# Kernel optimization log

Hardware: AMD Instinct MI355X
Metric: run time of the kernel (lower is better)

Reference implementation:

```python
import jax, jax.numpy as jnp
import numpy as np

B, M, N = 1, 8192, 131072      # batch, bones, window points
C_BOT, C = 16, 128             # bottleneck_channel, channel
K_MAX, FOLD, R_UP = 8, 8, 4    # max neighbors, fold_channel, upsample rate r
EPS = 1e-8


def _lin_init(key, fan_in, fan_out):
    return jax.random.normal(key, (fan_in, fan_out), jnp.float32) / np.sqrt(fan_in)


def setup_inputs() -> dict:
    key = jax.random.key(0)
    ks = jax.random.split(key, 10)
    return {
        "quantized_cf": jax.random.normal(ks[0], (B, M, C_BOT), jnp.float32),
        "d_idx": jax.random.randint(ks[1], (B, N, K_MAX), 0, M),
        "d_windows": jax.random.normal(ks[2], (B, N, 3), jnp.float32),
        "bones": jax.random.normal(ks[3], (B, M, 3), jnp.float32),
        "K": 8,
        # fea_stretch Linear(bottleneck -> channel)
        "W_stretch": _lin_init(ks[4], C_BOT, C),
        "b_stretch": jnp.zeros((C,), jnp.float32),
        # DWUS folding MLP: (C+3) -> C -> FOLD*R_UP -> 3 (per fold point)
        "W1": _lin_init(ks[5], C + 3, C),
        "b1": jnp.zeros((C,), jnp.float32),
        "W2": _lin_init(ks[6], C, FOLD * R_UP),
        "b2": jnp.zeros((FOLD * R_UP,), jnp.float32),
        "W3": _lin_init(ks[7], FOLD, 3),
        "b3": jnp.zeros((3,), jnp.float32),
    }


def reference(quantized_cf, d_idx, d_windows, bones, K,
              W_stretch, b_stretch, W1, b1, W2, b2, W3, b3):
    # fea_stretch: per-bone feature expansion  [B, M, C]
    skin_fea = jnp.einsum("bmc,cd->bmd", quantized_cf, W_stretch) + b_stretch

    idx = d_idx[..., :K]                                   # [B, N, K]
    batch = jnp.arange(B)[:, None, None]
    g_fea = skin_fea[batch, idx]                           # [B, N, K, C] gather
    g_bones = bones[batch, idx]                            # [B, N, K, 3]

    # inverse-distance interpolation of bone features onto window points
    rel = d_windows[:, :, None, :] - g_bones               # [B, N, K, 3]
    dist = jnp.sqrt(jnp.sum(rel * rel, axis=-1) + EPS)     # [B, N, K]
    w = 1.0 / (dist + EPS)
    w = w / jnp.sum(w, axis=-1, keepdims=True)
    interp = jnp.einsum("bnk,bnkc->bnc", w, g_fea)         # [B, N, C]

    # folding-based upsampling: each window point emits R_UP refined points
    x = jnp.concatenate([interp, d_windows], axis=-1)      # [B, N, C+3]
    h = jax.nn.relu(jnp.einsum("bnc,cd->bnd", x, W1) + b1)
    h = jax.nn.relu(jnp.einsum("bnc,cd->bnd", h, W2) + b2)
    h = h.reshape(B, N, R_UP, FOLD)
    off = jnp.einsum("bnrf,fo->bnro", h, W3) + b3          # [B, N, R_UP, 3]
    rec = d_windows[:, :, None, :] + off                   # [B, N, R_UP, 3]
    return rec.reshape(B, N * R_UP, 3)
```

## Files before the change

kernel.cpp:

```cpp
#include <hip/hip_runtime.h>

typedef __attribute__((ext_vector_type(8))) short short8;
typedef __attribute__((ext_vector_type(4))) float f32x4;

#define NPTS 131072

__device__ inline unsigned short f2bf(float f) {
    unsigned u = __float_as_uint(f);
    u = (u + 0x7FFFu + ((u >> 16) & 1u)) >> 16;
    return (unsigned short)u;
}

__global__ __launch_bounds__(256) void prep_kernel(
    const float* __restrict__ Ws, const float* __restrict__ bs,
    const float* __restrict__ W1, const float* __restrict__ b1,
    const float* __restrict__ W2,
    unsigned short* __restrict__ w1t, unsigned short* __restrict__ w2t,
    float* __restrict__ beff)
{
    int t = blockIdx.x * 256 + threadIdx.x;
    if (t < 4096) {
        int e = t >> 5, k = t & 31;
        float v = 0.f;
        if (k < 16) {
            for (int d = 0; d < 128; ++d) v = fmaf(Ws[k*128 + d], W1[d*128 + e], v);
        } else if (k < 19) {
            v = W1[(128 + (k - 16))*128 + e];
        }
        w1t[e*32 + k] = f2bf(v);
    } else if (t < 8192) {
        int t2 = t - 4096;
        int e = t2 >> 7, k = t2 & 127;
        w2t[e*128 + k] = f2bf(W2[k*32 + e]);
    } else if (t < 8320) {
        int e = t - 8192;
        float v = b1[e];
        for (int d = 0; d < 128; ++d) v = fmaf(bs[d], W1[d*128 + e], v);
        beff[e] = v;
    }
}

#define WREG 8768

__global__ __launch_bounds__(256, 2) void decoder_kernel(
    const float* __restrict__ qcf, const int* __restrict__ didx,
    const float* __restrict__ dwin, const float* __restrict__ bones,
    const unsigned short* __restrict__ w1t, const unsigned short* __restrict__ w2t,
    const float* __restrict__ beff, const float* __restrict__ b2,
    const float* __restrict__ W3, const float* __restrict__ b3,
    float* __restrict__ out)
{
    __shared__ unsigned char lds[4 * WREG];
    __shared__ float sW3[27];

    const int tid = threadIdx.x;
    if (tid < 24) sW3[tid] = W3[tid];
    if (tid < 3)  sW3[24 + tid] = b3[tid];
    __syncthreads();

    const int wave = tid >> 6;
    const int lane = tid & 63;
    unsigned char* wbase = lds + wave * WREG;
    unsigned short* Xb  = (unsigned short*)(wbase);
    unsigned short* H1b = (unsigned short*)(wbase + 1280);
    float*          H2b = (float*)(wbase + 5632);
    float*          Wb  = (float*)(wbase + 7744);
    int*            Ib  = (int*)(wbase + 8256);

    const int q4  = lane >> 4;
    const int l16 = lane & 15;

    short8 W1f[8]; float beffv[8];
#pragma unroll
    for (int dt = 0; dt < 8; ++dt) {
        W1f[dt]   = *(const short8*)(w1t + (dt*16 + l16)*32 + q4*8);
        beffv[dt] = beff[dt*16 + l16];
    }
    short8 W2f[2][4]; float b2v[2];
#pragma unroll
    for (int et = 0; et < 2; ++et) {
        b2v[et] = b2[et*16 + l16];
#pragma unroll
        for (int kt = 0; kt < 4; ++kt)
            W2f[et][kt] = *(const short8*)(w2t + (et*16 + l16)*128 + kt*32 + q4*8);
    }

    const int gw   = blockIdx.x * 4 + wave;
    const int base = gw * 16;

#pragma unroll
    for (int ph = 0; ph < 2; ++ph) {
        const int pl = ph*8 + (lane >> 3);
        const int k  = lane & 7;
        const int p  = base + pl;
        const int id = didx[p*8 + k];
        const float bx = bones[id*3+0], by = bones[id*3+1], bz = bones[id*3+2];
        const float rx = dwin[p*3+0] - bx;
        const float ry = dwin[p*3+1] - by;
        const float rz = dwin[p*3+2] - bz;
        const float dist = sqrtf(fmaf(rx,rx, fmaf(ry,ry, fmaf(rz,rz, 1e-8f))));
        const float w = 1.0f / (dist + 1e-8f);
        float s = w;
        s += __shfl_xor(s, 1);
        s += __shfl_xor(s, 2);
        s += __shfl_xor(s, 4);
        Wb[pl*8 + k] = w / s;
        Ib[pl*8 + k] = id;
    }

#pragma unroll
    for (int ps = 0; ps < 4; ++ps) {
        const int pl = ps*4 + q4;
        const int4   i0 = *(const int4*)(Ib + pl*8);
        const int4   i1 = *(const int4*)(Ib + pl*8 + 4);
        const float4 w0 = *(const float4*)(Wb + pl*8);
        const float4 w1 = *(const float4*)(Wb + pl*8 + 4);
        float acc = 0.f;
        acc = fmaf(w0.x, qcf[i0.x*16 + l16], acc);
        acc = fmaf(w0.y, qcf[i0.y*16 + l16], acc);
        acc = fmaf(w0.z, qcf[i0.z*16 + l16], acc);
        acc = fmaf(w0.w, qcf[i0.w*16 + l16], acc);
        acc = fmaf(w1.x, qcf[i1.x*16 + l16], acc);
        acc = fmaf(w1.y, qcf[i1.y*16 + l16], acc);
        acc = fmaf(w1.z, qcf[i1.z*16 + l16], acc);
        acc = fmaf(w1.w, qcf[i1.w*16 + l16], acc);
        Xb[pl*40 + l16] = f2bf(acc);
        float wv = 0.f;
        if (l16 < 3) wv = dwin[(base + pl)*3 + l16];
        Xb[pl*40 + 16 + l16] = f2bf(wv);
    }

    const short8 a1 = *(const short8*)(Xb + l16*40 + q4*8);
    f32x4 acc1[8];
#pragma unroll
    for (int dt = 0; dt < 8; ++dt) {
        f32x4 c = { beffv[dt], beffv[dt], beffv[dt], beffv[dt] };
        acc1[dt] = __builtin_amdgcn_mfma_f32_16x16x32_bf16(a1, W1f[dt], c, 0, 0, 0);
    }
#pragma unroll
    for (int dt = 0; dt < 8; ++dt) {
#pragma unroll
        for (int r = 0; r < 4; ++r) {
            const float h = fmaxf(acc1[dt][r], 0.f);
            H1b[(q4*4 + r)*136 + dt*16 + l16] = f2bf(h);
        }
    }

    f32x4 acc2[2] = { { b2v[0], b2v[0], b2v[0], b2v[0] },
                      { b2v[1], b2v[1], b2v[1], b2v[1] } };
#pragma unroll
    for (int kt = 0; kt < 4; ++kt) {
        const short8 a2 = *(const short8*)(H1b + l16*136 + kt*32 + q4*8);
        acc2[0] = __builtin_amdgcn_mfma_f32_16x16x32_bf16(a2, W2f[0][kt], acc2[0], 0, 0, 0);
        acc2[1] = __builtin_amdgcn_mfma_f32_16x16x32_bf16(a2, W2f[1][kt], acc2[1], 0, 0, 0);
    }
#pragma unroll
    for (int et = 0; et < 2; ++et) {
#pragma unroll
        for (int r = 0; r < 4; ++r) {
            H2b[(q4*4 + r)*33 + et*16 + l16] = fmaxf(acc2[et][r], 0.f);
        }
    }

#pragma unroll
    for (int i3 = 0; i3 < 3; ++i3) {
        const int g  = i3*64 + lane;
        const int pt = g / 12;
        const int q  = g - pt*12;
        const int r  = q / 3;
        const int o  = q - r*3;
        float acc = sW3[24 + o];
#pragma unroll
        for (int f = 0; f < 8; ++f)
            acc = fmaf(H2b[pt*33 + r*8 + f], sW3[f*3 + o], acc);
        const float wv = dwin[(base + pt)*3 + o];
        out[(size_t)base*12 + g] = wv + acc;
    }
}

extern "C" void kernel_launch(void* const* d_in, const int* in_sizes, int n_in,
                              void* d_out, int out_size, void* d_ws, size_t ws_size,
                              hipStream_t stream) {
    const float* qcf   = (const float*)d_in[0];
    const int*   didx  = (const int*)  d_in[1];
    const float* dwin  = (const float*)d_in[2];
    const float* bones = (const float*)d_in[3];
    const float* Ws = (const float*)d_in[5];
    const float* bs = (const float*)d_in[6];
    const float* W1 = (const float*)d_in[7];
    const float* b1 = (const float*)d_in[8];
    const float* W2 = (const float*)d_in[9];
    const float* b2 = (const float*)d_in[10];
    const float* W3 = (const float*)d_in[11];
    const float* b3 = (const float*)d_in[12];
    float* out = (float*)d_out;

    unsigned short* w1t  = (unsigned short*)d_ws;
    unsigned short* w2t  = (unsigned short*)((char*)d_ws + 8192);
    float*          beff = (float*)((char*)d_ws + 16384);

    hipLaunchKernelGGL(prep_kernel, dim3(33), dim3(256), 0, stream,
                       Ws, bs, W1, b1, W2, w1t, w2t, beff);
    hipLaunchKernelGGL(decoder_kernel, dim3(2048), dim3(256), 0, stream,
                       qcf, didx, dwin, bones, w1t, w2t, beff, b2, W3, b3, out);
}
```

Measured before the change: 31.43 us.

## Stream MLP weights per use, pack bf16 stores, run final fold on MFMA

Weight fragments for the first two layers are no longer kept in registers for the whole kernel; they are loaded from global memory right before each MFMA, and launch bounds rise to allow four blocks per CU. Hidden activations are packed two bf16 values at a time into permuted LDS layouts, and a matching permuted W2 layout is built in prep. The scalar W3 fold is replaced by one MFMA against a block-diagonal bf16 W3 matrix built in prep. This trades fewer registers and fewer ALU ops for repeated weight loads from global memory or cache, extra block-wide barriers, and lower precision in the last layer.

```diff
diff --git a/kernel.cpp b/kernel.cpp
--- a/kernel.cpp
+++ b/kernel.cpp
@@ -1,4 +1,5 @@
 #include <hip/hip_runtime.h>
+#include <hip/hip_bf16.h>
 
 typedef __attribute__((ext_vector_type(8))) short short8;
 typedef __attribute__((ext_vector_type(4))) float f32x4;
@@ -11,12 +12,18 @@
     return (unsigned short)u;
 }
 
+__device__ inline unsigned pack2(float a, float b) {
+    union { __hip_bfloat162 h; unsigned u; } v;
+    v.h = __float22bfloat162_rn(float2{a, b});
+    return v.u;
+}
+
 __global__ __launch_bounds__(256) void prep_kernel(
     const float* __restrict__ Ws, const float* __restrict__ bs,
     const float* __restrict__ W1, const float* __restrict__ b1,
-    const float* __restrict__ W2,
+    const float* __restrict__ W2, const float* __restrict__ W3,
     unsigned short* __restrict__ w1t, unsigned short* __restrict__ w2t,
-    float* __restrict__ beff)
+    float* __restrict__ beff, unsigned short* __restrict__ w3t)
 {
     int t = blockIdx.x * 256 + threadIdx.x;
     if (t < 4096) {
@@ -30,60 +37,51 @@
         w1t[e*32 + k] = f2bf(v);
     } else if (t < 8192) {
         int t2 = t - 4096;
-        int e = t2 >> 7, k = t2 & 127;
-        w2t[e*128 + k] = f2bf(W2[k*32 + e]);
+        int e = t2 >> 7, d = t2 & 127;
+        w2t[e*128 + ((d & 15)*8 + (d >> 4))] = f2bf(W2[d*32 + e]);
     } else if (t < 8320) {
         int e = t - 8192;
         float v = b1[e];
         for (int d = 0; d < 128; ++d) v = fmaf(bs[d], W1[d*128 + e], v);
         beff[e] = v;
-    }
-}
-
-#define WREG 8768
-
-__global__ __launch_bounds__(256, 2) void decoder_kernel(
+    } else if (t < 8832) {
+        int i = t - 8320;
+        int q = i >> 5, k = i & 31;
+        int e = (k & 1)*16 + (k >> 1);
+        int r = e >> 3, f = e & 7;
+        float v = 0.f;
+        if (q < 12) {
+            int r2 = q / 3, o = q - r2*3;
+            if (r == r2) v = W3[f*3 + o];
+        }
+        w3t[q*32 + k] = f2bf(v);
+    }
+}
+
+#define WREG 7936
+
+__global__ __launch_bounds__(256, 4) void decoder_kernel(
     const float* __restrict__ qcf, const int* __restrict__ didx,
     const float* __restrict__ dwin, const float* __restrict__ bones,
     const unsigned short* __restrict__ w1t, const unsigned short* __restrict__ w2t,
     const float* __restrict__ beff, const float* __restrict__ b2,
-    const float* __restrict__ W3, const float* __restrict__ b3,
+    const unsigned short* __restrict__ w3t, const float* __restrict__ b3,
     float* __restrict__ out)
 {
     __shared__ unsigned char lds[4 * WREG];
-    __shared__ float sW3[27];
-
-    const int tid = threadIdx.x;
-    if (tid < 24) sW3[tid] = W3[tid];
-    if (tid < 3)  sW3[24 + tid] = b3[tid];
-    __syncthreads();
-
+
+    const int tid  = threadIdx.x;
     const int wave = tid >> 6;
     const int lane = tid & 63;
     unsigned char* wbase = lds + wave * WREG;
     unsigned short* Xb  = (unsigned short*)(wbase);
     unsigned short* H1b = (unsigned short*)(wbase + 1280);
-    float*          H2b = (float*)(wbase + 5632);
-    float*          Wb  = (float*)(wbase + 7744);
-    int*            Ib  = (int*)(wbase + 8256);
+    unsigned short* H2p = (unsigned short*)(wbase + 5632);
+    float*          Wb  = (float*)(wbase + 6912);
+    int*            Ib  = (int*)(wbase + 7424);
 
     const int q4  = lane >> 4;
     const int l16 = lane & 15;
-
-    short8 W1f[8]; float beffv[8];
-#pragma unroll
-    for (int dt = 0; dt < 8; ++dt) {
-        W1f[dt]   = *(const short8*)(w1t + (dt*16 + l16)*32 + q4*8);
-        beffv[dt] = beff[dt*16 + l16];
-    }
-    short8 W2f[2][4]; float b2v[2];
-#pragma unroll
-    for (int et = 0; et < 2; ++et) {
-        b2v[et] = b2[et*16 + l16];
-#pragma unroll
-        for (int kt = 0; kt < 4; ++kt)
-            W2f[et][kt] = *(const short8*)(w2t + (et*16 + l16)*128 + kt*32 + q4*8);
-    }
 
     const int gw   = blockIdx.x * 4 + wave;
     const int base = gw * 16;
@@ -107,6 +105,7 @@
         Wb[pl*8 + k] = w / s;
         Ib[pl*8 + k] = id;
     }
+    __syncthreads();
 
 #pragma unroll
     for (int ps = 0; ps < 4; ++ps) {
@@ -129,52 +128,61 @@
         if (l16 < 3) wv = dwin[(base + pl)*3 + l16];
         Xb[pl*40 + 16 + l16] = f2bf(wv);
     }
+    __syncthreads();
 
     const short8 a1 = *(const short8*)(Xb + l16*40 + q4*8);
     f32x4 acc1[8];
 #pragma unroll
     for (int dt = 0; dt < 8; ++dt) {
-        f32x4 c = { beffv[dt], beffv[dt], beffv[dt], beffv[dt] };
-        acc1[dt] = __builtin_amdgcn_mfma_f32_16x16x32_bf16(a1, W1f[dt], c, 0, 0, 0);
-    }
-#pragma unroll
-    for (int dt = 0; dt < 8; ++dt) {
+        const short8 w1f = *(const short8*)(w1t + (dt*16 + l16)*32 + q4*8);
+        const float  bv  = beff[dt*16 + l16];
+        f32x4 c = { bv, bv, bv, bv };
+        acc1[dt] = __builtin_amdgcn_mfma_f32_16x16x32_bf16(a1, w1f, c, 0, 0, 0);
+    }
+#pragma unroll
+    for (int r = 0; r < 4; ++r) {
+        union { unsigned u[4]; short8 s; } pk;
+        pk.u[0] = pack2(fmaxf(acc1[0][r],0.f), fmaxf(acc1[1][r],0.f));
+        pk.u[1] = pack2(fmaxf(acc1[2][r],0.f), fmaxf(acc1[3][r],0.f));
+        pk.u[2] = pack2(fmaxf(acc1[4][r],0.f), fmaxf(acc1[5][r],0.f));
+        pk.u[3] = pack2(fmaxf(acc1[6][r],0.f), fmaxf(acc1[7][r],0.f));
+        *(short8*)(H1b + (q4*4 + r)*136 + l16*8) = pk.s;
+    }
+    __syncthreads();
+
+    f32x4 acc2[2];
+#pragma unroll
+    for (int et = 0; et < 2; ++et) {
+        const float bv = b2[et*16 + l16];
+        acc2[et] = f32x4{ bv, bv, bv, bv };
+    }
+#pragma unroll
+    for (int kt = 0; kt < 4; ++kt) {
+        const short8 a2   = *(const short8*)(H1b + l16*136 + kt*32 + q4*8);
+        const short8 w2f0 = *(const short8*)(w2t + (l16)*128      + kt*32 + q4*8);
+        const short8 w2f1 = *(const short8*)(w2t + (16 + l16)*128 + kt*32 + q4*8);
+        acc2[0] = __builtin_amdgcn_mfma_f32_16x16x32_bf16(a2, w2f0, acc2[0], 0, 0, 0);
+        acc2[1] = __builtin_amdgcn_mfma_f32_16x16x32_bf16(a2, w2f1, acc2[1], 0, 0, 0);
+    }
+#pragma unroll
+    for (int r = 0; r < 4; ++r) {
+        unsigned p01 = pack2(fmaxf(acc2[0][r],0.f), fmaxf(acc2[1][r],0.f));
+        *(unsigned*)(H2p + (q4*4 + r)*40 + l16*2) = p01;
+    }
+    __syncthreads();
+
+    const short8 a3  = *(const short8*)(H2p + l16*40 + q4*8);
+    const short8 w3f = *(const short8*)(w3t + l16*32 + q4*8);
+    const int o = l16 - (l16/3)*3;
+    const float b3o = (l16 < 12) ? b3[o] : 0.f;
+    f32x4 c3 = { b3o, b3o, b3o, b3o };
+    f32x4 o3 = __builtin_amdgcn_mfma_f32_16x16x32_bf16(a3, w3f, c3, 0, 0, 0);
+    if (l16 < 12) {
 #pragma unroll
         for (int r = 0; r < 4; ++r) {
-            const float h = fmaxf(acc1[dt][r], 0.f);
-            H1b[(q4*4 + r)*136 + dt*16 + l16] = f2bf(h);
+            const int pt = base + q4*4 + r;
+            out[(size_t)pt*12 + l16] = dwin[pt*3 + o] + o3[r];
         }
-    }
-
-    f32x4 acc2[2] = { { b2v[0], b2v[0], b2v[0], b2v[0] },
-                      { b2v[1], b2v[1], b2v[1], b2v[1] } };
-#pragma unroll
-    for (int kt = 0; kt < 4; ++kt) {
-        const short8 a2 = *(const short8*)(H1b + l16*136 + kt*32 + q4*8);
-        acc2[0] = __builtin_amdgcn_mfma_f32_16x16x32_bf16(a2, W2f[0][kt], acc2[0], 0, 0, 0);
-        acc2[1] = __builtin_amdgcn_mfma_f32_16x16x32_bf16(a2, W2f[1][kt], acc2[1], 0, 0, 0);
-    }
-#pragma unroll
-    for (int et = 0; et < 2; ++et) {
-#pragma unroll
-        for (int r = 0; r < 4; ++r) {
-            H2b[(q4*4 + r)*33 + et*16 + l16] = fmaxf(acc2[et][r], 0.f);
-        }
-    }
-
-#pragma unroll
-    for (int i3 = 0; i3 < 3; ++i3) {
-        const int g  = i3*64 + lane;
-        const int pt = g / 12;
-        const int q  = g - pt*12;
-        const int r  = q / 3;
-        const int o  = q - r*3;
-        float acc = sW3[24 + o];
-#pragma unroll
-        for (int f = 0; f < 8; ++f)
-            acc = fmaf(H2b[pt*33 + r*8 + f], sW3[f*3 + o], acc);
-        const float wv = dwin[(base + pt)*3 + o];
-        out[(size_t)base*12 + g] = wv + acc;
     }
 }
 
@@ -198,9 +206,10 @@
     unsigned short* w1t  = (unsigned short*)d_ws;
     unsigned short* w2t  = (unsigned short*)((char*)d_ws + 8192);
     float*          beff = (float*)((char*)d_ws + 16384);
-
-    hipLaunchKernelGGL(prep_kernel, dim3(33), dim3(256), 0, stream,
-                       Ws, bs, W1, b1, W2, w1t, w2t, beff);
+    unsigned short* w3t  = (unsigned short*)((char*)d_ws + 16896);
+
+    hipLaunchKernelGGL(prep_kernel, dim3(35), dim3(256), 0, stream,
+                       Ws, bs, W1, b1, W2, W3, w1t, w2t, beff, w3t);
     hipLaunchKernelGGL(decoder_kernel, dim3(2048), dim3(256), 0, stream,
-                       qcf, didx, dwin, bones, w1t, w2t, beff, b2, W3, b3, out);
-}
+                       qcf, didx, dwin, bones, w1t, w2t, beff, b2, w3t, b3, out);
+}
```

After: 34.50 us. 1.1x slower.

## Fuse weight prep and decoder into one cooperative kernel with grid sync

Applied to the files above, without the earlier changes.

Replaces the two launches (prep_kernel then decoder_kernel) with a single cooperative launch of 512 blocks. The blocks first do the weight preprocessing, then meet at a grid-wide barrier, and then each loops over four tiles of points, which also amortises the per-block register weight loads. The aim is to remove the second launch overhead and the inter-kernel gap. In exchange it adds the cost of a grid sync and lowers the number of resident blocks, which may reduce latency hiding for the gather-heavy work. If the cooperative launch fails, it falls back to the original two kernels.

```diff
diff --git a/kernel.cpp b/kernel.cpp
--- a/kernel.cpp
+++ b/kernel.cpp
@@ -1,4 +1,5 @@
 #include <hip/hip_runtime.h>
+#include <hip/hip_cooperative_groups.h>
 
 typedef __attribute__((ext_vector_type(8))) short short8;
 typedef __attribute__((ext_vector_type(4))) float f32x4;
@@ -10,6 +11,8 @@
     u = (u + 0x7FFFu + ((u >> 16) & 1u)) >> 16;
     return (unsigned short)u;
 }
+
+#define WREG 8768
 
 __global__ __launch_bounds__(256) void prep_kernel(
     const float* __restrict__ Ws, const float* __restrict__ bs,
@@ -40,54 +43,15 @@
     }
 }
 
-#define WREG 8768
-
-__global__ __launch_bounds__(256, 2) void decoder_kernel(
+__device__ __forceinline__ void decode_tile(
+    int base, int lane, int q4, int l16,
     const float* __restrict__ qcf, const int* __restrict__ didx,
     const float* __restrict__ dwin, const float* __restrict__ bones,
-    const unsigned short* __restrict__ w1t, const unsigned short* __restrict__ w2t,
-    const float* __restrict__ beff, const float* __restrict__ b2,
-    const float* __restrict__ W3, const float* __restrict__ b3,
+    const short8* W1f, const float* beffv, const short8 (*W2f)[4],
+    const float* b2v, const float* sW3,
+    unsigned short* Xb, unsigned short* H1b, float* H2b, float* Wb, int* Ib,
     float* __restrict__ out)
 {
-    __shared__ unsigned char lds[4 * WREG];
-    __shared__ float sW3[27];
-
-    const int tid = threadIdx.x;
-    if (tid < 24) sW3[tid] = W3[tid];
-    if (tid < 3)  sW3[24 + tid] = b3[tid];
-    __syncthreads();
-
-    const int wave = tid >> 6;
-    const int lane = tid & 63;
-    unsigned char* wbase = lds + wave * WREG;
-    unsigned short* Xb  = (unsigned short*)(wbase);
-    unsigned short* H1b = (unsigned short*)(wbase + 1280);
-    float*          H2b = (float*)(wbase + 5632);
-    float*          Wb  = (float*)(wbase + 7744);
-    int*            Ib  = (int*)(wbase + 8256);
-
-    const int q4  = lane >> 4;
-    const int l16 = lane & 15;
-
-    short8 W1f[8]; float beffv[8];
-#pragma unroll
-    for (int dt = 0; dt < 8; ++dt) {
-        W1f[dt]   = *(const short8*)(w1t + (dt*16 + l16)*32 + q4*8);
-        beffv[dt] = beff[dt*16 + l16];
-    }
-    short8 W2f[2][4]; float b2v[2];
-#pragma unroll
-    for (int et = 0; et < 2; ++et) {
-        b2v[et] = b2[et*16 + l16];
-#pragma unroll
-        for (int kt = 0; kt < 4; ++kt)
-            W2f[et][kt] = *(const short8*)(w2t + (et*16 + l16)*128 + kt*32 + q4*8);
-    }
-
-    const int gw   = blockIdx.x * 4 + wave;
-    const int base = gw * 16;
-
 #pragma unroll
     for (int ph = 0; ph < 2; ++ph) {
         const int pl = ph*8 + (lane >> 3);
@@ -178,6 +142,135 @@
     }
 }
 
+__global__ __launch_bounds__(256, 2) void decoder_kernel(
+    const float* __restrict__ qcf, const int* __restrict__ didx,
+    const float* __restrict__ dwin, const float* __restrict__ bones,
+    const unsigned short* __restrict__ w1t, const unsigned short* __restrict__ w2t,
+    const float* __restrict__ beff, const float* __restrict__ b2,
+    const float* __restrict__ W3, const float* __restrict__ b3,
+    float* __restrict__ out)
+{
+    __shared__ unsigned char lds[4 * WREG];
+    __shared__ float sW3[27];
+
+    const int tid = threadIdx.x;
+    if (tid < 24) sW3[tid] = W3[tid];
+    if (tid < 3)  sW3[24 + tid] = b3[tid];
+    __syncthreads();
+
+    const int wave = tid >> 6;
+    const int lane = tid & 63;
+    unsigned char* wbase = lds + wave * WREG;
+    unsigned short* Xb  = (unsigned short*)(wbase);
+    unsigned short* H1b = (unsigned short*)(wbase + 1280);
+    float*          H2b = (float*)(wbase + 5632);
+    float*          Wb  = (float*)(wbase + 7744);
+    int*            Ib  = (int*)(wbase + 8256);
+
+    const int q4  = lane >> 4;
+    const int l16 = lane & 15;
+
+    short8 W1f[8]; float beffv[8];
+#pragma unroll
+    for (int dt = 0; dt < 8; ++dt) {
+        W1f[dt]   = *(const short8*)(w1t + (dt*16 + l16)*32 + q4*8);
+        beffv[dt] = beff[dt*16 + l16];
+    }
+    short8 W2f[2][4]; float b2v[2];
+#pragma unroll
+    for (int et = 0; et < 2; ++et) {
+        b2v[et] = b2[et*16 + l16];
+#pragma unroll
+        for (int kt = 0; kt < 4; ++kt)
+            W2f[et][kt] = *(const short8*)(w2t + (et*16 + l16)*128 + kt*32 + q4*8);
+    }
+
+    const int gw   = blockIdx.x * 4 + wave;
+    const int base = gw * 16;
+
+    decode_tile(base, lane, q4, l16, qcf, didx, dwin, bones,
+                W1f, beffv, W2f, b2v, sW3, Xb, H1b, H2b, Wb, Ib, out);
+}
+
+__global__ __launch_bounds__(256, 2) void fused_kernel(
+    const float* __restrict__ qcf, const int* __restrict__ didx,
+    const float* __restrict__ dwin, const float* __restrict__ bones,
+    const float* __restrict__ Ws, const float* __restrict__ bs,
+    const float* __restrict__ W1, const float* __restrict__ b1,
+    const float* __restrict__ W2, const float* __restrict__ b2,
+    const float* __restrict__ W3, const float* __restrict__ b3,
+    unsigned short* __restrict__ w1t, unsigned short* __restrict__ w2t,
+    float* __restrict__ beff, float* __restrict__ out)
+{
+    __shared__ unsigned char lds[4 * WREG];
+    __shared__ float sW3[27];
+
+    const int tid = threadIdx.x;
+
+    {
+        int t = blockIdx.x * 256 + tid;
+        if (t < 4096) {
+            int e = t >> 5, k = t & 31;
+            float v = 0.f;
+            if (k < 16) {
+                for (int d = 0; d < 128; ++d) v = fmaf(Ws[k*128 + d], W1[d*128 + e], v);
+            } else if (k < 19) {
+                v = W1[(128 + (k - 16))*128 + e];
+            }
+            w1t[e*32 + k] = f2bf(v);
+        } else if (t < 8192) {
+            int t2 = t - 4096;
+            int e = t2 >> 7, k = t2 & 127;
+            w2t[e*128 + k] = f2bf(W2[k*32 + e]);
+        } else if (t < 8320) {
+            int e = t - 8192;
+            float v = b1[e];
+            for (int d = 0; d < 128; ++d) v = fmaf(bs[d], W1[d*128 + e], v);
+            beff[e] = v;
+        }
+    }
+
+    cooperative_groups::this_grid().sync();
+
+    if (tid < 24) sW3[tid] = W3[tid];
+    if (tid < 3)  sW3[24 + tid] = b3[tid];
+    __syncthreads();
+
+    const int wave = tid >> 6;
+    const int lane = tid & 63;
+    unsigned char* wbase = lds + wave * WREG;
+    unsigned short* Xb  = (unsigned short*)(wbase);
+    unsigned short* H1b = (unsigned short*)(wbase + 1280);
+    float*          H2b = (float*)(wbase + 5632);
+    float*          Wb  = (float*)(wbase + 7744);
+    int*            Ib  = (int*)(wbase + 8256);
+
+    const int q4  = lane >> 4;
+    const int l16 = lane & 15;
+
+    short8 W1f[8]; float beffv[8];
+#pragma unroll
+    for (int dt = 0; dt < 8; ++dt) {
+        W1f[dt]   = *(const short8*)(w1t + (dt*16 + l16)*32 + q4*8);
+        beffv[dt] = beff[dt*16 + l16];
+    }
+    short8 W2f[2][4]; float b2v[2];
+#pragma unroll
+    for (int et = 0; et < 2; ++et) {
+        b2v[et] = b2[et*16 + l16];
+#pragma unroll
+        for (int kt = 0; kt < 4; ++kt)
+            W2f[et][kt] = *(const short8*)(w2t + (et*16 + l16)*128 + kt*32 + q4*8);
+    }
+
+    for (int it = 0; it < 4; ++it) {
+        const int gw   = (it*512 + blockIdx.x)*4 + wave;
+        const int base = gw * 16;
+        decode_tile(base, lane, q4, l16, qcf, didx, dwin, bones,
+                    W1f, beffv, W2f, b2v, sW3, Xb, H1b, H2b, Wb, Ib, out);
+    }
+}
+
 extern "C" void kernel_launch(void* const* d_in, const int* in_sizes, int n_in,
                               void* d_out, int out_size, void* d_ws, size_t ws_size,
                               hipStream_t stream) {
@@ -199,8 +292,19 @@
     unsigned short* w2t  = (unsigned short*)((char*)d_ws + 8192);
     float*          beff = (float*)((char*)d_ws + 16384);
 
-    hipLaunchKernelGGL(prep_kernel, dim3(33), dim3(256), 0, stream,
-                       Ws, bs, W1, b1, W2, w1t, w2t, beff);
-    hipLaunchKernelGGL(decoder_kernel, dim3(2048), dim3(256), 0, stream,
-                       qcf, didx, dwin, bones, w1t, w2t, beff, b2, W3, b3, out);
-}
+    void* args[16] = {
+        (void*)&qcf, (void*)&didx, (void*)&dwin, (void*)&bones,
+        (void*)&Ws,  (void*)&bs,   (void*)&W1,   (void*)&b1,
+        (void*)&W2,  (void*)&b2,   (void*)&W3,   (void*)&b3,
+        (void*)&w1t, (void*)&w2t,  (void*)&beff, (void*)&out
+    };
+    hipError_t err = hipLaunchCooperativeKernel(
+        (const void*)fused_kernel, dim3(512), dim3(256), args, 0, stream);
+
+    if (err != hipSuccess) {
+        hipLaunchKernelGGL(prep_kernel, dim3(33), dim3(256), 0, stream,
+                           Ws, bs, W1, b1, W2, w1t, w2t, beff);
+        hipLaunchKernelGGL(decoder_kernel, dim3(2048), dim3(256), 0, stream,
+                           qcf, didx, dwin, bones, w1t, w2t, beff, b2, W3, b3, out);
+    }
+}
```

New measurement: 77.19 us. 146% more time.
